# Optimization experiments

Hardware: AMD Instinct MI355X
Metric: run time of the kernel (lower is better)

The kernel has to match this reference:

```python
import jax, jax.numpy as jnp
import numpy as np

NCLS = 21
HW = 41  # featUpsample target size


def setup_inputs() -> dict:
    key = jax.random.key(0)
    ks = jax.random.split(key, 8)
    x = jax.random.normal(ks[0], (4, 2048, 33, 33), dtype=jnp.float32)
    diffW = jax.random.uniform(ks[1], (4, HW * HW, HW * HW), dtype=jnp.float32)
    # conv weights init normal(0, 0.01) as in the torch module
    conv_w = jax.random.normal(ks[2], (1024, 2048, 3, 3), dtype=jnp.float32) * 0.01
    conv_b = jnp.zeros((1024,), jnp.float32)
    cls_w = jax.random.normal(ks[3], (NCLS, 1024, 1, 1), dtype=jnp.float32) * 0.01
    cls_b = jnp.zeros((NCLS,), jnp.float32)
    sm_scale_w = jnp.ones((1, NCLS), jnp.float32) * 1.5   # softMax_scale.weights
    pool_w = jnp.ones((1, NCLS), jnp.float32) * 5.0       # weiPooling.weights
    ms_scales = jnp.array([0.95, 0.75, 0.6, 0.4], jnp.float32)
    return {"x": x, "diffW": diffW, "conv_w": conv_w, "conv_b": conv_b,
            "cls_w": cls_w, "cls_b": cls_b, "sm_scale_w": sm_scale_w,
            "pool_w": pool_w, "ms_scales": ms_scales}


def reference(x, diffW, conv_w, conv_b, cls_w, cls_b, sm_scale_w, pool_w, ms_scales):
    bs = x.shape[0]
    # bilinear upsample to 41x41 (align_corners=False semantics, same as jax.image.resize)
    x = jax.image.resize(x, (bs, x.shape[1], HW, HW), method="bilinear")
    # ASPP branch 0: dilated 3x3 conv, dilation=padding=6 keeps 41x41
    feat = jax.lax.conv_general_dilated(
        x, conv_w, window_strides=(1, 1), padding=((6, 6), (6, 6)),
        rhs_dilation=(6, 6), dimension_numbers=("NCHW", "OIHW", "NCHW"))
    feat = feat + conv_b[None, :, None, None]          # [bs,1024,41,41]
    d = feat.shape[1]
    wh = HW * HW
    f2 = feat.reshape(bs, d, wh)                        # [bs,1024,wh]
    cw = cls_w.reshape(NCLS, d)                         # 1x1 conv weight

    logits = []
    for it in range(4):
        cs = (diffW > ms_scales[it]).astype(f2.dtype)   # [bs,wh,wh]
        # diag(1/rowsum) @ cs, then transpose -> column-normalized-after-transpose
        norm = (cs / cs.sum(axis=2, keepdims=True)).transpose(0, 2, 1)
        od = jnp.einsum("bdn,bnm->bdm", f2, norm)       # diffusion-smoothed features
        logits.append(jnp.einsum("bdm,cd->bcm", od, cw) + cls_b[None, :, None])
    wei_cum = jnp.stack(logits, axis=1)                 # [bs,4,ncls,wh]

    # softMax_scale: softmax over the scale (ns) axis of scaled logits
    wei_mask = jax.nn.softmax(sm_scale_w.reshape(1, 1, NCLS, 1) * wei_cum, axis=1)
    wei_cum2 = jax.nn.softmax((wei_cum * wei_mask).sum(axis=1), axis=1)  # [bs,ncls,wh]

    # weiPooling
    wei = jax.nn.softmax(wei_cum2, axis=1)
    w2 = jax.nn.softmax(wei * jnp.exp(pool_w[0]).reshape(1, NCLS, 1), axis=2)
    pooled = jnp.einsum("bcm,bdm->bcd", w2, f2)         # [bs,ncls,1024]

    # pred_sw with the 1x1 classifier weights
    out = (pooled * cw[None]).sum(axis=2) + cls_b[None]  # [bs,ncls]
    prob = jax.nn.sigmoid(out).reshape(bs, 1, NCLS)
    return (prob, wei_cum2, wei, wei_mask)
```

## Files before the change

kernel.cpp:

```cpp
#include <hip/hip_runtime.h>
#include <hip/hip_bf16.h>
#include <math.h>

#define NCLS 21
#define WH 1681
#define WHP 1684
#define BS 4
#define CIN 2048
#define NSRC 1089
#define KPOS 18432
#define MR 192
#define HS 836352
#define NT 53
#define NZ 8
#define PSLAB (16L * 22L * WHP)
#define MKZ 4
#define MSLAB (32L * KPOS)

typedef __attribute__((ext_vector_type(8))) __bf16 bf16x8;
typedef __attribute__((ext_vector_type(4))) float f32x4;

#define WS_KC    393216L
#define WS_H2    393248L
#define WS_WCUM  (WS_H2 + 4L * HS)
#define WS_G     (WS_WCUM + 564816L)
#define WS_GSW   (WS_G + 141204L)
#define WS_CF    (WS_GSW + 108544L)
#define WS_W2P   (WS_CF + 591712L)
#define WS_W2MB  (WS_W2P + 6193152L)

static __device__ __forceinline__ unsigned short f2bf(float v) {
    unsigned int b = __float_as_uint(v);
    b += 0x7FFFu + ((b >> 16) & 1u);
    return (unsigned short)(b >> 16);
}


__global__ void k_prep(const float* __restrict__ clsw, const float* __restrict__ convb,
                       const float* __restrict__ clsb, unsigned short* __restrict__ cf,
                       float* __restrict__ Kc) {
    if (blockIdx.x < 16) {
        int gid = blockIdx.x * 256 + threadIdx.x;
        int lane = gid & 63;
        int rt = (gid >> 6) & 1;
        int kc = gid >> 7;
        int cl = lane & 15, kg = lane >> 4;
        int c = rt * 16 + cl;
        unsigned short o[8];
#pragma unroll
        for (int j = 0; j < 8; ++j) {
            int d = kc * 32 + kg * 8 + j;
            o[j] = (c < NCLS) ? f2bf(clsw[c * 1024 + d]) : (unsigned short)0;
        }
        unsigned short* p = cf + (long)gid * 8;
#pragma unroll
        for (int j = 0; j < 8; ++j) p[j] = o[j];
    } else {
        __shared__ float red[256];
        int c = blockIdx.x - 16;
        float s = 0.f;
        for (int d = threadIdx.x; d < 1024; d += 256) s += clsw[c * 1024 + d] * convb[d];
        red[threadIdx.x] = s; __syncthreads();
        for (int o = 128; o > 0; o >>= 1) {
            if (threadIdx.x < o) red[threadIdx.x] += red[threadIdx.x + o];
            __syncthreads();
        }
        if (threadIdx.x == 0) Kc[c] = red[0] + clsb[c];
    }
}

#define LOADC(dst, ch) { const float* cc_ = cb + (long)((ch) * 32 + wv * 8) * KPOS; \
    _Pragma("unroll") for (int jj = 0; jj < 8; ++jj) dst[jj] = cc_[(long)jj * KPOS]; }

__global__ __launch_bounds__(256) void k_mergemm(const unsigned short* __restrict__ cf,
                                                 const float* __restrict__ convw,
                                                 float* __restrict__ pmrg) {
    __shared__ unsigned short Bs[2][64][40];
    int tid = threadIdx.x;
    int lane = tid & 63, wv = tid >> 6;
    int kg = lane >> 4, cl = lane & 15;
    int pos0 = blockIdx.x * 64;
    int kz = blockIdx.y;

    const float* cb = convw + (long)(kz * 256) * KPOS + pos0 + lane;

    f32x4 acc[2];
#pragma unroll
    for (int i = 0; i < 2; ++i) acc[i] = (f32x4){0.f, 0.f, 0.f, 0.f};

    float xr0[8], xr1[8], xrn[8];
    LOADC(xr0, 0);
    LOADC(xr1, 1);
    for (int ch = 0; ch < 8; ++ch) {
        if (ch + 2 < 8) LOADC(xrn, ch + 2);
        bf16x8 afr[2];
        const unsigned short* ab = cf + (((long)(kz * 8 + ch) * 2) * 64 + lane) * 8;
#pragma unroll
        for (int i = 0; i < 2; ++i) afr[i] = *(const bf16x8*)(ab + (long)i * 64 * 8);
        union { unsigned short u[8]; bf16x8 v; } bw;
#pragma unroll
        for (int jj = 0; jj < 8; ++jj) bw.u[jj] = f2bf(xr0[jj]);
        int buf = ch & 1;
        *(bf16x8*)&Bs[buf][lane][wv * 8] = bw.v;
        __syncthreads();
        bf16x8 bf = *(const bf16x8*)&Bs[buf][wv * 16 + cl][kg * 8];
#pragma unroll
        for (int i = 0; i < 2; ++i)
            acc[i] = __builtin_amdgcn_mfma_f32_16x16x32_bf16(afr[i], bf, acc[i], 0, 0, 0);
#pragma unroll
        for (int jj = 0; jj < 8; ++jj) { xr0[jj] = xr1[jj]; xr1[jj] = xrn[jj]; }
    }
    float* pz = pmrg + (long)kz * MSLAB;
    int pos = pos0 + wv * 16 + cl;
#pragma unroll
    for (int i = 0; i < 2; ++i) {
#pragma unroll
        for (int rr = 0; rr < 4; ++rr) {
            int c = i * 16 + 4 * kg + rr;
            pz[(long)c * KPOS + pos] = acc[i][rr];
        }
    }
}

__global__ void k_mfinpack(const float* __restrict__ pmrg, unsigned short* __restrict__ w2mb) {
    int gid = blockIdx.x * blockDim.x + threadIdx.x;
    if (gid >= 64 * 12 * 64) return;
    int lane = gid & 63;
    int rt = (gid >> 6) % 12;
    int kc = gid / (64 * 12);
    int cl = lane & 15, kg = lane >> 4;
    int r = rt * 16 + cl;
    unsigned short o[8];
    if (r < 189) {
        int c = r / 9, t = r - c * 9;
        const float* base = pmrg + (long)c * KPOS + t;
#pragma unroll
        for (int j = 0; j < 8; ++j) {
            int i = kc * 32 + kg * 8 + j;
            long pos = (long)i * 9;
            float s = 0.f;
#pragma unroll
            for (int kz = 0; kz < MKZ; ++kz) s += base[(long)kz * MSLAB + pos];
            o[j] = f2bf(s);
        }
    } else {
#pragma unroll
        for (int j = 0; j < 8; ++j) o[j] = 0;
    }
    unsigned short* p = w2mb + (long)gid * 8;
#pragma unroll
    for (int j = 0; j < 8; ++j) p[j] = o[j];
}

#define LOADX(dst, ch) { const float* xc_ = xb + (long)((ch) * 32 + wv * 8) * NSRC; \
    _Pragma("unroll") for (int jj = 0; jj < 8; ++jj) dst[jj] = nok ? xc_[(long)jj * NSRC] : 0.f; }

__global__ __launch_bounds__(256) void k_gemmm(const unsigned short* __restrict__ w2mb,
                                               const float* __restrict__ x,
                                               float* __restrict__ Hp) {
    __shared__ unsigned short Bs[2][64][40];
    int tid = threadIdx.x;
    int lane = tid & 63, wv = tid >> 6;
    int kg = lane >> 4, cl = lane & 15;
    int n0 = blockIdx.x * 64;
    int b  = blockIdx.y;
    int ks = blockIdx.z;

    const float* xb = x + ((long)b * CIN + ks * 512) * NSRC + n0 + lane;
    bool nok = (n0 + lane) < NSRC;

    f32x4 acc[3][4];
#pragma unroll
    for (int i = 0; i < 3; ++i)
#pragma unroll
        for (int ct = 0; ct < 4; ++ct) acc[i][ct] = (f32x4){0.f, 0.f, 0.f, 0.f};

    float xr0[8], xr1[8], xrn[8];
    LOADX(xr0, 0);
    LOADX(xr1, 1);
    for (int ch = 0; ch < 16; ++ch) {
        if (ch + 2 < 16) LOADX(xrn, ch + 2);
        bf16x8 afr[3];
        const unsigned short* wb = w2mb + (((long)(ks * 16 + ch) * 12 + wv * 3) * 64 + lane) * 8;
#pragma unroll
        for (int i = 0; i < 3; ++i) afr[i] = *(const bf16x8*)(wb + (long)i * 64 * 8);
        union { unsigned short u[8]; bf16x8 v; } bw;
#pragma unroll
        for (int jj = 0; jj < 8; ++jj) bw.u[jj] = f2bf(xr0[jj]);
        int buf = ch & 1;
        *(bf16x8*)&Bs[buf][lane][wv * 8] = bw.v;
        __syncthreads();
#pragma unroll
        for (int ct = 0; ct < 4; ++ct) {
            bf16x8 bf = *(const bf16x8*)&Bs[buf][ct * 16 + cl][kg * 8];
#pragma unroll
            for (int i = 0; i < 3; ++i)
                acc[i][ct] = __builtin_amdgcn_mfma_f32_16x16x32_bf16(afr[i], bf, acc[i][ct], 0, 0, 0);
        }
#pragma unroll
        for (int jj = 0; jj < 8; ++jj) { xr0[jj] = xr1[jj]; xr1[jj] = xrn[jj]; }
    }
    float* Hb = Hp + (long)ks * HS + (long)b * MR * NSRC;
#pragma unroll
    for (int i = 0; i < 3; ++i) {
        int r0 = (wv * 3 + i) * 16 + 4 * kg;
#pragma unroll
        for (int ct = 0; ct < 4; ++ct) {
            int n = n0 + ct * 16 + cl;
            if (n < NSRC) {
#pragma unroll
                for (int rr = 0; rr < 4; ++rr)
                    Hb[(long)(r0 + rr) * NSRC + n] = acc[i][ct][rr];
            }
        }
    }
}

__global__ void k_combine(const float* __restrict__ Hp, float* __restrict__ g) {
    int gid = blockIdx.x * blockDim.x + threadIdx.x;
    if (gid >= BS * NCLS * WH) return;
    int m = gid % WH;
    int t_ = gid / WH;
    int c = t_ % NCLS;
    int b = t_ / NCLS;
    int yy = m / 41, xx = m - yy * 41;
    const float S = 33.0f / 41.0f;
    int y0a[3], y1a[3], x0a[3], x1a[3];
    float wya[3], wxa[3];
    bool oky[3], okx[3];
#pragma unroll
    for (int o = 0; o < 3; ++o) {
        int yp = yy + 6 * o - 6;
        oky[o] = (yp >= 0 && yp < 41);
        float sy = (yp + 0.5f) * S - 0.5f;
        float fy = floorf(sy);
        wya[o] = sy - fy;
        int y0 = (int)fy;
        y0a[o] = min(max(y0, 0), 32);
        y1a[o] = min(max(y0 + 1, 0), 32);
        int xp = xx + 6 * o - 6;
        okx[o] = (xp >= 0 && xp < 41);
        float sx = (xp + 0.5f) * S - 0.5f;
        float fx = floorf(sx);
        wxa[o] = sx - fx;
        int x0 = (int)fx;
        x0a[o] = min(max(x0, 0), 32);
        x1a[o] = min(max(x0 + 1, 0), 32);
    }
    float acc = 0.f;
    const float* Hb = Hp + ((long)b * MR + c * 9) * NSRC;
#pragma unroll
    for (int ty = 0; ty < 3; ++ty) {
#pragma unroll
        for (int tx = 0; tx < 3; ++tx) {
            if (oky[ty] && okx[tx]) {
                const float* hr = Hb + (ty * 3 + tx) * NSRC;
                int i00 = y0a[ty] * 33 + x0a[tx], i01 = y0a[ty] * 33 + x1a[tx];
                int i10 = y1a[ty] * 33 + x0a[tx], i11 = y1a[ty] * 33 + x1a[tx];
                float v00 = 0.f, v01 = 0.f, v10 = 0.f, v11 = 0.f;
#pragma unroll
                for (int s = 0; s < 4; ++s) {
                    const float* h2 = hr + (long)s * HS;
                    v00 += h2[i00]; v01 += h2[i01]; v10 += h2[i10]; v11 += h2[i11];
                }
                float wy = wya[ty], wx = wxa[tx];
                float v0 = v00 + wx * (v01 - v00);
                float v1 = v10 + wx * (v11 - v10);
                acc += v0 + wy * (v1 - v0);
            }
        }
    }
    g[gid] = acc;
}

__global__ void k_gpack(const float* __restrict__ g, unsigned short* __restrict__ Gsw) {
    int gid = blockIdx.x * blockDim.x + threadIdx.x;
    if (gid >= BS * NT * 2 * 64) return;
    int lane = gid & 63;
    int t = gid >> 6;
    int ct = t & 1; t >>= 1;
    int nt = t % NT;
    int b  = t / NT;
    int col = ct * 16 + (lane & 15);
    int nb = nt * 32 + (lane >> 4) * 8;
    unsigned short out[8];
#pragma unroll
    for (int j = 0; j < 8; ++j) {
        int n = nb + j;
        unsigned short v = 0;
        if (n < WH) {
            if (col < NCLS) v = f2bf(g[((long)b * NCLS + col) * WH + n]);
            else if (col == NCLS) v = 0x3F80;
        }
        out[j] = v;
    }
    unsigned short* p = Gsw + (long)gid * 8;
#pragma unroll
    for (int j = 0; j < 8; ++j) p[j] = out[j];
}

__global__ __launch_bounds__(256) void k_dgemm(const float* __restrict__ diffW,
                                               const unsigned short* __restrict__ Gsw,
                                               const float* __restrict__ msc,
                                               float* __restrict__ pacc) {
    __shared__ float Ds[2][64][36];
    int tid  = threadIdx.x;
    int lane = tid & 63, wv = tid >> 6;
    int b = blockIdx.y, z = blockIdx.z;
    int m0 = blockIdx.x * 64;
    int m0w = m0 + wv * 16;
    int kg = lane >> 4;
    int cl = lane & 15;
    float thr[4];
#pragma unroll
    for (int it = 0; it < 4; ++it) thr[it] = msc[it];
    int nt0 = (z * NT) / NZ;
    int nt1 = ((z + 1) * NT) / NZ;

    int scol = tid & 31;
    int srow = tid >> 5;
    long rb[8];
#pragma unroll
    for (int p = 0; p < 8; ++p) {
        int mr = m0 + srow + 8 * p; if (mr > WH - 1) mr = WH - 1;
        rb[p] = ((long)b * WH + mr) * WH;
    }
    const unsigned short* gb = Gsw + (long)b * NT * 2 * 64 * 8;

    f32x4 accv[4][2];
#pragma unroll
    for (int it = 0; it < 4; ++it)
#pragma unroll
        for (int ct = 0; ct < 2; ++ct) accv[it][ct] = (f32x4){0.f, 0.f, 0.f, 0.f};

    for (int nt = nt0; nt < nt1; ++nt) {
        int nb = nt * 32;
        int buf = nt & 1;
        int ncol = nb + scol;
        if (ncol <= WH - 1) {
#pragma unroll
            for (int p = 0; p < 8; ++p) Ds[buf][srow + 8 * p][scol] = diffW[rb[p] + ncol];
        } else {
#pragma unroll
            for (int p = 0; p < 8; ++p) Ds[buf][srow + 8 * p][scol] = -1e30f;
        }
        __syncthreads();

        float dw[8];
        const float* dsr = &Ds[buf][wv * 16 + cl][kg * 8];
#pragma unroll
        for (int j = 0; j < 8; ++j) dw[j] = dsr[j];

        union { unsigned short u[8]; bf16x8 v; } af[4];
#pragma unroll
        for (int it = 0; it < 4; ++it)
#pragma unroll
            for (int j = 0; j < 8; ++j)
                af[it].u[j] = (dw[j] > thr[it]) ? (unsigned short)0x3F80 : (unsigned short)0;

        const unsigned short* gp = gb + ((long)nt * 2 * 64 + lane) * 8;
        bf16x8 b0 = *(const bf16x8*)gp;
        bf16x8 b1 = *(const bf16x8*)(gp + 64 * 8);
#pragma unroll
        for (int it = 0; it < 4; ++it) {
            accv[it][0] = __builtin_amdgcn_mfma_f32_16x16x32_bf16(af[it].v, b0, accv[it][0], 0, 0, 0);
            accv[it][1] = __builtin_amdgcn_mfma_f32_16x16x32_bf16(af[it].v, b1, accv[it][1], 0, 0, 0);
        }
    }
    float* pz = pacc + (long)z * PSLAB;
    int mbase = m0w + 4 * kg;
#pragma unroll
    for (int it = 0; it < 4; ++it) {
#pragma unroll
        for (int ct = 0; ct < 2; ++ct) {
            int c = ct * 16 + cl;
            if (c < 22) {
                float* dst = pz + ((long)(b * 4 + it) * 22 + c) * WHP + mbase;
                if (mbase + 3 < WH) {
                    *(f32x4*)dst = accv[it][ct];
                } else {
#pragma unroll
                    for (int r = 0; r < 4; ++r)
                        if (mbase + r < WH) dst[r] = accv[it][ct][r];
                }
            }
        }
    }
}

__global__ void k_dfin(const float* __restrict__ pacc, const float* __restrict__ Kc,
                       float* __restrict__ wcum) {
    int gid = blockIdx.x * blockDim.x + threadIdx.x;
    if (gid >= BS * 4 * NCLS * WH) return;
    int m = gid % WH;
    int t = gid / WH;
    int c = t % NCLS; t /= NCLS;
    int it = t & 3;
    int b = t >> 2;
    long rowc = ((long)(b * 4 + it) * 22 + c) * WHP + m;
    long rown = ((long)(b * 4 + it) * 22 + NCLS) * WHP + m;
    float num = 0.f, cnt = 0.f;
#pragma unroll
    for (int z = 0; z < NZ; ++z) {
        num += pacc[(long)z * PSLAB + rowc];
        cnt += pacc[(long)z * PSLAB + rown];
    }
    wcum[(((long)b * 4 + it) * NCLS + c) * WH + m] = num / cnt + Kc[c];
}

__global__ void k_mask(const float* __restrict__ wcum, const float* __restrict__ smw,
                       float* __restrict__ out_wc2, float* __restrict__ out_wei,
                       float* __restrict__ out_mask) {
    int gid = blockIdx.x * blockDim.x + threadIdx.x;
    if (gid >= BS * WH) return;
    int b = gid / WH, m = gid - b * WH;
    const float* base = wcum + (long)b * 4 * NCLS * WH + m;

    float fused[21];
#pragma unroll
    for (int c = 0; c < NCLS; ++c) {
        float sc = smw[c];
        float L0 = base[(0 * NCLS + c) * WH];
        float L1 = base[(1 * NCLS + c) * WH];
        float L2 = base[(2 * NCLS + c) * WH];
        float L3 = base[(3 * NCLS + c) * WH];
        float a0 = sc * L0, a1 = sc * L1, a2 = sc * L2, a3 = sc * L3;
        float mx = fmaxf(fmaxf(a0, a1), fmaxf(a2, a3));
        float e0 = __expf(a0 - mx), e1 = __expf(a1 - mx), e2 = __expf(a2 - mx), e3 = __expf(a3 - mx);
        float inv = 1.0f / (e0 + e1 + e2 + e3);
        e0 *= inv; e1 *= inv; e2 *= inv; e3 *= inv;
        out_mask[((long)(b * 4 + 0) * NCLS + c) * WH + m] = e0;
        out_mask[((long)(b * 4 + 1) * NCLS + c) * WH + m] = e1;
        out_mask[((long)(b * 4 + 2) * NCLS + c) * WH + m] = e2;
        out_mask[((long)(b * 4 + 3) * NCLS + c) * WH + m] = e3;
        fused[c] = L0 * e0 + L1 * e1 + L2 * e2 + L3 * e3;
    }
    float mx = -1e30f;
#pragma unroll
    for (int c = 0; c < NCLS; ++c) mx = fmaxf(mx, fused[c]);
    float s = 0.f;
    float e[21];
#pragma unroll
    for (int c = 0; c < NCLS; ++c) { e[c] = __expf(fused[c] - mx); s += e[c]; }
    float inv = 1.0f / s;
#pragma unroll
    for (int c = 0; c < NCLS; ++c) {
        e[c] *= inv;
        out_wc2[((long)b * NCLS + c) * WH + m] = e[c];
    }
    mx = -1e30f;
#pragma unroll
    for (int c = 0; c < NCLS; ++c) mx = fmaxf(mx, e[c]);
    s = 0.f;
    float e2a[21];
#pragma unroll
    for (int c = 0; c < NCLS; ++c) { e2a[c] = __expf(e[c] - mx); s += e2a[c]; }
    inv = 1.0f / s;
#pragma unroll
    for (int c = 0; c < NCLS; ++c) out_wei[((long)b * NCLS + c) * WH + m] = e2a[c] * inv;
}

__global__ void k_pool(const float* __restrict__ wei, const float* __restrict__ g,
                       const float* __restrict__ poolw, const float* __restrict__ Kc,
                       float* __restrict__ prob) {
    int c = blockIdx.x, b = blockIdx.y;
    const float* wr = wei + ((long)b * NCLS + c) * WH;
    const float* gr = g + ((long)b * NCLS + c) * WH;
    float E = __expf(poolw[c]);
    __shared__ float red[256];
    float mx = -1e30f;
    for (int m = threadIdx.x; m < WH; m += 256) mx = fmaxf(mx, wr[m] * E);
    red[threadIdx.x] = mx; __syncthreads();
    for (int o = 128; o > 0; o >>= 1) {
        if (threadIdx.x < o) red[threadIdx.x] = fmaxf(red[threadIdx.x], red[threadIdx.x + o]);
        __syncthreads();
    }
    mx = red[0]; __syncthreads();
    float se = 0.f, sg = 0.f;
    for (int m = threadIdx.x; m < WH; m += 256) {
        float ev = __expf(wr[m] * E - mx);
        se += ev; sg += ev * gr[m];
    }
    red[threadIdx.x] = se; __syncthreads();
    for (int o = 128; o > 0; o >>= 1) {
        if (threadIdx.x < o) red[threadIdx.x] += red[threadIdx.x + o];
        __syncthreads();
    }
    se = red[0]; __syncthreads();
    red[threadIdx.x] = sg; __syncthreads();
    for (int o = 128; o > 0; o >>= 1) {
        if (threadIdx.x < o) red[threadIdx.x] += red[threadIdx.x + o];
        __syncthreads();
    }
    sg = red[0];
    if (threadIdx.x == 0) {
        float out = sg / se + Kc[c];
        prob[b * NCLS + c] = 1.0f / (1.0f + __expf(-out));
    }
}

extern "C" void kernel_launch(void* const* d_in, const int* in_sizes, int n_in,
                              void* d_out, int out_size, void* d_ws, size_t ws_size,
                              hipStream_t stream) {
    const float* x      = (const float*)d_in[0];
    const float* diffW  = (const float*)d_in[1];
    const float* conv_w = (const float*)d_in[2];
    const float* conv_b = (const float*)d_in[3];
    const float* cls_w  = (const float*)d_in[4];
    const float* cls_b  = (const float*)d_in[5];
    const float* smw    = (const float*)d_in[6];
    const float* poolw  = (const float*)d_in[7];
    const float* msc    = (const float*)d_in[8];

    float* ws   = (float*)d_ws;
    float* Kc   = ws + WS_KC;
    float* Hp   = ws + WS_H2;
    float* wcum = ws + WS_WCUM;
    float* g    = ws + WS_G;
    unsigned short* Gsw  = (unsigned short*)(ws + WS_GSW);
    unsigned short* cf   = (unsigned short*)(ws + WS_CF);
    float* pmrg = ws + WS_W2P;
    float* pacc = ws + WS_W2P;
    unsigned short* w2mb = (unsigned short*)(ws + WS_W2MB);

    float* out  = (float*)d_out;
    float* o_prob = out;
    float* o_wc2  = out + 84;
    float* o_wei  = out + 84 + 141204;
    float* o_mask = out + 84 + 141204 + 141204;

    k_prep<<<37, 256, 0, stream>>>(cls_w, conv_b, cls_b, cf, Kc);
    k_mergemm<<<dim3(KPOS / 64, MKZ), 256, 0, stream>>>(cf, conv_w, pmrg);
    k_mfinpack<<<(64 * 12 * 64 + 255) / 256, 256, 0, stream>>>(pmrg, w2mb);
    k_gemmm<<<dim3(18, BS, 4), 256, 0, stream>>>(w2mb, x, Hp);
    k_combine<<<(BS * NCLS * WH + 255) / 256, 256, 0, stream>>>(Hp, g);
    k_gpack<<<(BS * NT * 2 * 64 + 255) / 256, 256, 0, stream>>>(g, Gsw);
    k_dgemm<<<dim3(27, BS, NZ), 256, 0, stream>>>(diffW, Gsw, msc, pacc);
    k_dfin<<<(BS * 4 * NCLS * WH + 255) / 256, 256, 0, stream>>>(pacc, Kc, wcum);
    k_mask<<<(BS * WH + 63) / 64, 64, 0, stream>>>(wcum, smw, o_wc2, o_wei, o_mask);
    k_pool<<<dim3(NCLS, BS), 256, 0, stream>>>(o_wei, g, poolw, Kc, o_prob);
}
```

Measured before the change: 94.84 us.

## Remove prep kernel by folding weight packing and bias constant into consumers

Drops the separate k_prep launch. k_mergemm now reads cls_w directly and converts it to bf16 in-register, and the per-class bias constant Kc is recomputed inside k_mask (per block) and k_pool. This saves one kernel launch and a workspace round-trip. In exchange, each k_mask block redoes a 21x1024 dot-product reduction, which adds redundant work across about 106 blocks. The diffW GEMM split-K count also drops from 8 to 6, which cuts partial-sum traffic in k_dfin but gives k_dgemm fewer blocks to spread across the device.

```diff
diff --git a/kernel.cpp b/kernel.cpp
--- a/kernel.cpp
+++ b/kernel.cpp
@@ -12,7 +12,7 @@
 #define MR 192
 #define HS 836352
 #define NT 53
-#define NZ 8
+#define NZ 6
 #define PSLAB (16L * 22L * WHP)
 #define MKZ 4
 #define MSLAB (32L * KPOS)
@@ -20,13 +20,11 @@
 typedef __attribute__((ext_vector_type(8))) __bf16 bf16x8;
 typedef __attribute__((ext_vector_type(4))) float f32x4;
 
-#define WS_KC    393216L
 #define WS_H2    393248L
 #define WS_WCUM  (WS_H2 + 4L * HS)
 #define WS_G     (WS_WCUM + 564816L)
 #define WS_GSW   (WS_G + 141204L)
-#define WS_CF    (WS_GSW + 108544L)
-#define WS_W2P   (WS_CF + 591712L)
+#define WS_W2P   (WS_GSW + 108544L + 591712L)
 #define WS_W2MB  (WS_W2P + 6193152L)
 
 static __device__ __forceinline__ unsigned short f2bf(float v) {
@@ -35,44 +33,10 @@
     return (unsigned short)(b >> 16);
 }
 
-
-__global__ void k_prep(const float* __restrict__ clsw, const float* __restrict__ convb,
-                       const float* __restrict__ clsb, unsigned short* __restrict__ cf,
-                       float* __restrict__ Kc) {
-    if (blockIdx.x < 16) {
-        int gid = blockIdx.x * 256 + threadIdx.x;
-        int lane = gid & 63;
-        int rt = (gid >> 6) & 1;
-        int kc = gid >> 7;
-        int cl = lane & 15, kg = lane >> 4;
-        int c = rt * 16 + cl;
-        unsigned short o[8];
-#pragma unroll
-        for (int j = 0; j < 8; ++j) {
-            int d = kc * 32 + kg * 8 + j;
-            o[j] = (c < NCLS) ? f2bf(clsw[c * 1024 + d]) : (unsigned short)0;
-        }
-        unsigned short* p = cf + (long)gid * 8;
-#pragma unroll
-        for (int j = 0; j < 8; ++j) p[j] = o[j];
-    } else {
-        __shared__ float red[256];
-        int c = blockIdx.x - 16;
-        float s = 0.f;
-        for (int d = threadIdx.x; d < 1024; d += 256) s += clsw[c * 1024 + d] * convb[d];
-        red[threadIdx.x] = s; __syncthreads();
-        for (int o = 128; o > 0; o >>= 1) {
-            if (threadIdx.x < o) red[threadIdx.x] += red[threadIdx.x + o];
-            __syncthreads();
-        }
-        if (threadIdx.x == 0) Kc[c] = red[0] + clsb[c];
-    }
-}
-
 #define LOADC(dst, ch) { const float* cc_ = cb + (long)((ch) * 32 + wv * 8) * KPOS; \
     _Pragma("unroll") for (int jj = 0; jj < 8; ++jj) dst[jj] = cc_[(long)jj * KPOS]; }
 
-__global__ __launch_bounds__(256) void k_mergemm(const unsigned short* __restrict__ cf,
+__global__ __launch_bounds__(256) void k_mergemm(const float* __restrict__ clsw,
                                                  const float* __restrict__ convw,
                                                  float* __restrict__ pmrg) {
     __shared__ unsigned short Bs[2][64][40];
@@ -94,9 +58,22 @@
     for (int ch = 0; ch < 8; ++ch) {
         if (ch + 2 < 8) LOADC(xrn, ch + 2);
         bf16x8 afr[2];
-        const unsigned short* ab = cf + (((long)(kz * 8 + ch) * 2) * 64 + lane) * 8;
-#pragma unroll
-        for (int i = 0; i < 2; ++i) afr[i] = *(const bf16x8*)(ab + (long)i * 64 * 8);
+#pragma unroll
+        for (int i = 0; i < 2; ++i) {
+            int c = i * 16 + cl;
+            union { unsigned short u[8]; bf16x8 v; } aw;
+            if (c < NCLS) {
+                const float* cw = clsw + (long)c * 1024 + kz * 256 + ch * 32 + kg * 8;
+                float4 w0 = *(const float4*)cw;
+                float4 w1 = *(const float4*)(cw + 4);
+                aw.u[0] = f2bf(w0.x); aw.u[1] = f2bf(w0.y); aw.u[2] = f2bf(w0.z); aw.u[3] = f2bf(w0.w);
+                aw.u[4] = f2bf(w1.x); aw.u[5] = f2bf(w1.y); aw.u[6] = f2bf(w1.z); aw.u[7] = f2bf(w1.w);
+            } else {
+#pragma unroll
+                for (int j = 0; j < 8; ++j) aw.u[j] = 0;
+            }
+            afr[i] = aw.v;
+        }
         union { unsigned short u[8]; bf16x8 v; } bw;
 #pragma unroll
         for (int jj = 0; jj < 8; ++jj) bw.u[jj] = f2bf(xr0[jj]);
@@ -388,8 +365,7 @@
     }
 }
 
-__global__ void k_dfin(const float* __restrict__ pacc, const float* __restrict__ Kc,
-                       float* __restrict__ wcum) {
+__global__ void k_dfin(const float* __restrict__ pacc, float* __restrict__ wcum) {
     int gid = blockIdx.x * blockDim.x + threadIdx.x;
     if (gid >= BS * 4 * NCLS * WH) return;
     int m = gid % WH;
@@ -405,13 +381,29 @@
         num += pacc[(long)z * PSLAB + rowc];
         cnt += pacc[(long)z * PSLAB + rown];
     }
-    wcum[(((long)b * 4 + it) * NCLS + c) * WH + m] = num / cnt + Kc[c];
-}
-
-__global__ void k_mask(const float* __restrict__ wcum, const float* __restrict__ smw,
-                       float* __restrict__ out_wc2, float* __restrict__ out_wei,
-                       float* __restrict__ out_mask) {
-    int gid = blockIdx.x * blockDim.x + threadIdx.x;
+    wcum[(((long)b * 4 + it) * NCLS + c) * WH + m] = num / cnt;
+}
+
+__global__ __launch_bounds__(64) void k_mask(const float* __restrict__ wcum,
+                                             const float* __restrict__ smw,
+                                             const float* __restrict__ clsw,
+                                             const float* __restrict__ convb,
+                                             const float* __restrict__ clsb,
+                                             float* __restrict__ out_wc2,
+                                             float* __restrict__ out_wei,
+                                             float* __restrict__ out_mask) {
+    __shared__ float KcS[NCLS];
+    int lane = threadIdx.x;
+    for (int c = 0; c < NCLS; ++c) {
+        float s = 0.f;
+        for (int d = lane; d < 1024; d += 64) s += clsw[c * 1024 + d] * convb[d];
+#pragma unroll
+        for (int o = 1; o < 64; o <<= 1) s += __shfl_xor(s, o, 64);
+        if (lane == 0) KcS[c] = s + clsb[c];
+    }
+    __syncthreads();
+
+    int gid = blockIdx.x * 64 + lane;
     if (gid >= BS * WH) return;
     int b = gid / WH, m = gid - b * WH;
     const float* base = wcum + (long)b * 4 * NCLS * WH + m;
@@ -419,11 +411,12 @@
     float fused[21];
 #pragma unroll
     for (int c = 0; c < NCLS; ++c) {
+        float kc = KcS[c];
         float sc = smw[c];
-        float L0 = base[(0 * NCLS + c) * WH];
-        float L1 = base[(1 * NCLS + c) * WH];
-        float L2 = base[(2 * NCLS + c) * WH];
-        float L3 = base[(3 * NCLS + c) * WH];
+        float L0 = base[(0 * NCLS + c) * WH] + kc;
+        float L1 = base[(1 * NCLS + c) * WH] + kc;
+        float L2 = base[(2 * NCLS + c) * WH] + kc;
+        float L3 = base[(3 * NCLS + c) * WH] + kc;
         float a0 = sc * L0, a1 = sc * L1, a2 = sc * L2, a3 = sc * L3;
         float mx = fmaxf(fmaxf(a0, a1), fmaxf(a2, a3));
         float e0 = __expf(a0 - mx), e1 = __expf(a1 - mx), e2 = __expf(a2 - mx), e3 = __expf(a3 - mx);
@@ -461,7 +454,8 @@
 }
 
 __global__ void k_pool(const float* __restrict__ wei, const float* __restrict__ g,
-                       const float* __restrict__ poolw, const float* __restrict__ Kc,
+                       const float* __restrict__ poolw, const float* __restrict__ clsw,
+                       const float* __restrict__ convb, const float* __restrict__ clsb,
                        float* __restrict__ prob) {
     int c = blockIdx.x, b = blockIdx.y;
     const float* wr = wei + ((long)b * NCLS + c) * WH;
@@ -476,11 +470,12 @@
         __syncthreads();
     }
     mx = red[0]; __syncthreads();
-    float se = 0.f, sg = 0.f;
+    float se = 0.f, sg = 0.f, kcp = 0.f;
     for (int m = threadIdx.x; m < WH; m += 256) {
         float ev = __expf(wr[m] * E - mx);
         se += ev; sg += ev * gr[m];
     }
+    for (int d = threadIdx.x; d < 1024; d += 256) kcp += clsw[c * 1024 + d] * convb[d];
     red[threadIdx.x] = se; __syncthreads();
     for (int o = 128; o > 0; o >>= 1) {
         if (threadIdx.x < o) red[threadIdx.x] += red[threadIdx.x + o];
@@ -492,9 +487,15 @@
         if (threadIdx.x < o) red[threadIdx.x] += red[threadIdx.x + o];
         __syncthreads();
     }
-    sg = red[0];
+    sg = red[0]; __syncthreads();
+    red[threadIdx.x] = kcp; __syncthreads();
+    for (int o = 128; o > 0; o >>= 1) {
+        if (threadIdx.x < o) red[threadIdx.x] += red[threadIdx.x + o];
+        __syncthreads();
+    }
+    kcp = red[0];
     if (threadIdx.x == 0) {
-        float out = sg / se + Kc[c];
+        float out = sg / se + kcp + clsb[c];
         prob[b * NCLS + c] = 1.0f / (1.0f + __expf(-out));
     }
 }
@@ -513,12 +514,10 @@
     const float* msc    = (const float*)d_in[8];
 
     float* ws   = (float*)d_ws;
-    float* Kc   = ws + WS_KC;
     float* Hp   = ws + WS_H2;
     float* wcum = ws + WS_WCUM;
     float* g    = ws + WS_G;
     unsigned short* Gsw  = (unsigned short*)(ws + WS_GSW);
-    unsigned short* cf   = (unsigned short*)(ws + WS_CF);
     float* pmrg = ws + WS_W2P;
     float* pacc = ws + WS_W2P;
     unsigned short* w2mb = (unsigned short*)(ws + WS_W2MB);
@@ -529,14 +528,14 @@
     float* o_wei  = out + 84 + 141204;
     float* o_mask = out + 84 + 141204 + 141204;
 
-    k_prep<<<37, 256, 0, stream>>>(cls_w, conv_b, cls_b, cf, Kc);
-    k_mergemm<<<dim3(KPOS / 64, MKZ), 256, 0, stream>>>(cf, conv_w, pmrg);
+    k_mergemm<<<dim3(KPOS / 64, MKZ), 256, 0, stream>>>(cls_w, conv_w, pmrg);
     k_mfinpack<<<(64 * 12 * 64 + 255) / 256, 256, 0, stream>>>(pmrg, w2mb);
     k_gemmm<<<dim3(18, BS, 4), 256, 0, stream>>>(w2mb, x, Hp);
     k_combine<<<(BS * NCLS * WH + 255) / 256, 256, 0, stream>>>(Hp, g);
     k_gpack<<<(BS * NT * 2 * 64 + 255) / 256, 256, 0, stream>>>(g, Gsw);
     k_dgemm<<<dim3(27, BS, NZ), 256, 0, stream>>>(diffW, Gsw, msc, pacc);
-    k_dfin<<<(BS * 4 * NCLS * WH + 255) / 256, 256, 0, stream>>>(pacc, Kc, wcum);
-    k_mask<<<(BS * WH + 63) / 64, 64, 0, stream>>>(wcum, smw, o_wc2, o_wei, o_mask);
-    k_pool<<<dim3(NCLS, BS), 256, 0, stream>>>(o_wei, g, poolw, Kc, o_prob);
-}
+    k_dfin<<<(BS * 4 * NCLS * WH + 255) / 256, 256, 0, stream>>>(pacc, wcum);
+    k_mask<<<(BS * WH + 63) / 64, 64, 0, stream>>>(wcum, smw, cls_w, conv_b, cls_b,
+                                                   o_wc2, o_wei, o_mask);
+    k_pool<<<dim3(NCLS, BS), 256, 0, stream>>>(o_wei, g, poolw, cls_w, conv_b, cls_b, o_prob);
+}
```

After: 182.5 us. 1.92x slower.
